# Optimization experiments

Measured on AMD Instinct MI355X. Metric: run time of the kernel, lower is better.

Reference implementation:

```python
import jax, jax.numpy as jnp
from jax import lax
import numpy as np

VTH = 1.0  # config['v_threshold']

@jax.custom_vjp
def mg_spike(x):
    # forward of MultiGaussianSurrogate: Heaviside
    return (x > 0).astype(x.dtype)

def _mg_fwd(x):
    return mg_spike(x), x

def _mg_bwd(x, g):
    lens, scale, height, gamma = 0.5, 6.0, 0.15, 0.5
    def gaussian(v, mu, sigma):
        return jnp.exp(-(v - mu) ** 2 / (2.0 * sigma ** 2)) / jnp.sqrt(2.0 * jnp.pi) / sigma
    temp = (gaussian(x, 0.0, lens) * (1.0 + height)
            - gaussian(x, lens, scale * lens) * height
            - gaussian(x, -lens, scale * lens) * height)
    return (g * temp * gamma,)

mg_spike.defvjp(_mg_fwd, _mg_bwd)

def setup_inputs():
    key = jax.random.key(0)
    ks = jax.random.split(key, 6)
    B, T, D, H, O = 256, 250, 700, 1024, 35
    x = jax.random.normal(ks[0], (B, T, D), dtype=jnp.float32)
    W_dense = jax.random.normal(ks[1], (D, H), dtype=jnp.float32) / np.sqrt(D).astype(np.float32)
    b_dense = jnp.zeros((H,), dtype=jnp.float32)
    W_out = jax.random.normal(ks[2], (H, O), dtype=jnp.float32) / np.sqrt(H).astype(np.float32)
    b_out = jnp.zeros((O,), dtype=jnp.float32)
    tau_m = jax.random.uniform(ks[3], (H,), dtype=jnp.float32, minval=0.0, maxval=4.0)
    mem0 = jax.random.uniform(ks[4], (B, H), dtype=jnp.float32)
    spike0 = jax.random.uniform(ks[5], (B, H), dtype=jnp.float32)
    return {"x": x, "W_dense": W_dense, "b_dense": b_dense,
            "W_out": W_out, "b_out": b_out, "tau_m": tau_m,
            "mem0": mem0, "spike0": spike0}

def reference(x, W_dense, b_dense, W_out, b_out, tau_m, mem0, spike0):
    B, T, D = x.shape
    O = W_out.shape[1]
    alpha = jax.nn.sigmoid(tau_m)  # [H], constant over time
    # batch the input projection once: [B,T,H] -> scan over T
    d_all = jnp.einsum('btd,dh->bth', x, W_dense) + b_dense
    d_all = jnp.swapaxes(d_all, 0, 1)  # [T,B,H]

    def step(carry, inp):
        mem, spike, acc = carry
        d_input, i = inp
        mem = mem * alpha + (1.0 - alpha) * d_input - VTH * spike
        spike = mg_spike(mem - VTH)
        probs = jax.nn.softmax(spike @ W_out + b_out, axis=1)  # [B,O]
        acc = acc + jnp.where(i > 10, probs, jnp.zeros_like(probs))
        return (mem, spike, acc), None

    acc0 = jnp.zeros((B, O), dtype=x.dtype)
    (_, _, out), _ = lax.scan(step, (mem0, spike0, acc0), (d_all, jnp.arange(T)))
    return out
```

## Files before the change

### kernel.cpp

```cpp
#include <hip/hip_runtime.h>
#include <cstdint>
#include <cstddef>

#define B_ 256
#define T_ 250
#define D_ 700
#define KP 704
#define H_ 1024
#define O_ 35
#define NT 22
#define MPAD 256

typedef __attribute__((ext_vector_type(8))) short s16x8;
typedef __attribute__((ext_vector_type(4))) float fx4;

__device__ __forceinline__ unsigned short f2bf(float v) {
    union { float f; unsigned int u; } a; a.f = v;
    unsigned int r = a.u + 0x7FFFu + ((a.u >> 16) & 1u);
    return (unsigned short)(r >> 16);
}

__device__ __forceinline__ void glds16(const unsigned short* g, void* l) {
    __builtin_amdgcn_global_load_lds(
        (const __attribute__((address_space(1))) unsigned int*)(const void*)g,
        (__attribute__((address_space(3))) unsigned int*)l, 16, 0, 0);
}

__global__ __launch_bounds__(256)
void convW(const float* __restrict__ Wd, unsigned short* __restrict__ WhT,
           unsigned short* __restrict__ WlT)
{
    __shared__ float tile[32][33];
    const int tx = threadIdx.x, ty = threadIdx.y;
    const int bx = blockIdx.x, by = blockIdx.y;
#pragma unroll
    for (int i = 0; i < 4; ++i) {
        int k = by * 32 + ty + i * 8;
        int n = bx * 32 + tx;
        tile[ty + i * 8][tx] = (k < D_) ? Wd[(size_t)k * H_ + n] : 0.f;
    }
    __syncthreads();
#pragma unroll
    for (int i = 0; i < 4; ++i) {
        int n = bx * 32 + ty + i * 8;
        int k = by * 32 + tx;
        float v = tile[tx][ty + i * 8];
        unsigned short h = f2bf(v);
        union { unsigned int u; float f; } hf; hf.u = ((unsigned int)h) << 16;
        unsigned short lo = f2bf(v - hf.f);
        WhT[(size_t)n * KP + k] = h;
        WlT[(size_t)n * KP + k] = lo;
    }
}

__global__ __launch_bounds__(256)
void convX(const float* __restrict__ X, unsigned short* __restrict__ xh,
           unsigned short* __restrict__ xl)
{
    int idx = blockIdx.x * 256 + threadIdx.x;
    if (idx >= B_ * T_ * 88) return;
    int m = idx / 88, s = idx - m * 88;
    int k = s * 8;
    int b = m / T_, tt = m - b * T_;
    const float* row = X + (size_t)m * D_;
    float v[8];
#pragma unroll
    for (int j = 0; j < 4; ++j) v[j] = row[k + j];
    if (k + 4 < D_) {
#pragma unroll
        for (int j = 0; j < 4; ++j) v[4 + j] = row[k + 4 + j];
    } else {
#pragma unroll
        for (int j = 0; j < 4; ++j) v[4 + j] = 0.f;
    }
    unsigned int hw[4], lw[4];
#pragma unroll
    for (int j = 0; j < 4; ++j) {
        unsigned short h0 = f2bf(v[2 * j]), h1 = f2bf(v[2 * j + 1]);
        union { unsigned int u; float f; } a0, a1;
        a0.u = ((unsigned int)h0) << 16; a1.u = ((unsigned int)h1) << 16;
        unsigned short l0 = f2bf(v[2 * j] - a0.f), l1 = f2bf(v[2 * j + 1] - a1.f);
        hw[j] = (unsigned int)h0 | ((unsigned int)h1 << 16);
        lw[j] = (unsigned int)l0 | ((unsigned int)l1 << 16);
    }
    size_t drow = (size_t)(b * MPAD + tt) * KP + k;
    *reinterpret_cast<uint4*>(xh + drow) = make_uint4(hw[0], hw[1], hw[2], hw[3]);
    *reinterpret_cast<uint4*>(xl + drow) = make_uint4(lw[0], lw[1], lw[2], lw[3]);
}

__global__ __launch_bounds__(512, 2)
void gemm1(const unsigned short* __restrict__ Ahp, const unsigned short* __restrict__ Alp,
           const unsigned short* __restrict__ Bhp, const unsigned short* __restrict__ Blp,
           const float* __restrict__ bias, const float* __restrict__ tau,
           const float* __restrict__ mem0, const float* __restrict__ spk0,
           unsigned long long* __restrict__ bits)
{
    extern __shared__ char smem[];
    const int tid = threadIdx.x;
    const int l = tid & 63, w = tid >> 6;
    const int wm = w >> 2, wn = w & 3;

    const int nwg = gridDim.x, orig = blockIdx.x;
    const int xcd = orig & 7, idx = orig >> 3;
    const int q = nwg >> 3, r = nwg & 7;
    const int swz = (xcd < r ? xcd * (q + 1) : r * (q + 1) + (xcd - r) * q) + idx;
    const int by = swz >> 2, bx = swz & 3;
    const int m0 = by * MPAD, n0 = bx * 256;

    const int rr = tid >> 2, ss = tid & 3;
    const int sw8 = ((ss ^ ((rr >> 1) & 3)) << 3);
    const int offA = (m0 + rr) * KP + sw8;
    const int offB = (n0 + rr) * KP + sw8;
    const int wbase = w * 1024;

    const int ra0 = wm * 128 + (l & 15);
    const int rb0 = wn * 64 + (l & 15);
    const int aHb = ra0 * 64 + (((l >> 4) ^ ((ra0 >> 1) & 3)) << 4);
    const int bHb = rb0 * 64 + (((l >> 4) ^ ((rb0 >> 1) & 3)) << 4);

    fx4 acc[8][4];
#pragma unroll
    for (int i = 0; i < 8; ++i)
#pragma unroll
        for (int j = 0; j < 4; ++j) acc[i][j] = (fx4)0.f;

    auto stageA = [&](int buf, int t) {
        char* base = smem + buf * 65536 + wbase;
        const int k = t * 32;
        glds16(Ahp + offA + k, base);
        glds16(Ahp + offA + 128 * KP + k, base + 8192);
        glds16(Alp + offA + k, base + 16384);
        glds16(Alp + offA + 128 * KP + k, base + 24576);
    };
    auto stageB = [&](int buf, int t) {
        char* base = smem + buf * 65536 + 32768 + wbase;
        const int k = t * 32;
        glds16(Bhp + offB + k, base);
        glds16(Bhp + offB + 128 * KP + k, base + 8192);
        glds16(Blp + offB + k, base + 16384);
        glds16(Blp + offB + 128 * KP + k, base + 24576);
    };

    stageA(0, 0);
    stageB(0, 0);
    stageB(1, 1);
    asm volatile("s_waitcnt vmcnt(4)" ::: "memory");
    __builtin_amdgcn_s_barrier();

    for (int t = 0; t < NT; ++t) {
        const char* cb = smem + (t & 1) * 65536;
        s16x8 ah0[4], al0[4], ah1[4], al1[4], bh[4], bl[4];

#pragma unroll
        for (int f = 0; f < 4; ++f) {
            ah0[f] = *(const s16x8*)(cb + aHb + f * 1024);
            bh[f]  = *(const s16x8*)(cb + 32768 + bHb + f * 1024);
        }
        if (t + 1 < NT) stageA((t + 1) & 1, t + 1);

#pragma unroll
        for (int f = 0; f < 4; ++f) {
            al0[f] = *(const s16x8*)(cb + 16384 + aHb + f * 1024);
            bl[f]  = *(const s16x8*)(cb + 49152 + bHb + f * 1024);
        }
        __builtin_amdgcn_s_setprio(1);
#pragma unroll
        for (int fm = 0; fm < 4; ++fm)
#pragma unroll
            for (int fn = 0; fn < 4; ++fn)
                acc[fm][fn] = __builtin_amdgcn_mfma_f32_16x16x32_bf16(ah0[fm], bh[fn], acc[fm][fn], 0, 0, 0);
        __builtin_amdgcn_s_setprio(0);

#pragma unroll
        for (int f = 0; f < 4; ++f) {
            ah1[f] = *(const s16x8*)(cb + aHb + 4096 + f * 1024);
            al1[f] = *(const s16x8*)(cb + 16384 + aHb + 4096 + f * 1024);
        }
        __builtin_amdgcn_s_setprio(1);
#pragma unroll
        for (int fm = 0; fm < 4; ++fm)
#pragma unroll
            for (int fn = 0; fn < 4; ++fn) {
                acc[fm][fn] = __builtin_amdgcn_mfma_f32_16x16x32_bf16(ah0[fm], bl[fn], acc[fm][fn], 0, 0, 0);
                acc[fm][fn] = __builtin_amdgcn_mfma_f32_16x16x32_bf16(al0[fm], bh[fn], acc[fm][fn], 0, 0, 0);
            }
        __builtin_amdgcn_s_setprio(0);
        __builtin_amdgcn_sched_barrier(0);
        __builtin_amdgcn_s_barrier();

        if (t + 2 < NT) {
            stageB(t & 1, t + 2);
            asm volatile("s_waitcnt vmcnt(4)" ::: "memory");
        } else {
            asm volatile("s_waitcnt vmcnt(0)" ::: "memory");
        }

        __builtin_amdgcn_s_setprio(1);
#pragma unroll
        for (int fm = 0; fm < 4; ++fm)
#pragma unroll
            for (int fn = 0; fn < 4; ++fn)
                acc[fm + 4][fn] = __builtin_amdgcn_mfma_f32_16x16x32_bf16(ah1[fm], bh[fn], acc[fm + 4][fn], 0, 0, 0);
        __builtin_amdgcn_s_setprio(0);

        __builtin_amdgcn_s_setprio(1);
#pragma unroll
        for (int fm = 0; fm < 4; ++fm)
#pragma unroll
            for (int fn = 0; fn < 4; ++fn) {
                acc[fm + 4][fn] = __builtin_amdgcn_mfma_f32_16x16x32_bf16(ah1[fm], bl[fn], acc[fm + 4][fn], 0, 0, 0);
                acc[fm + 4][fn] = __builtin_amdgcn_mfma_f32_16x16x32_bf16(al1[fm], bh[fn], acc[fm + 4][fn], 0, 0, 0);
            }
        __builtin_amdgcn_s_setprio(0);
        __builtin_amdgcn_sched_barrier(0);
        __builtin_amdgcn_s_barrier();
    }

    float bv[4];
#pragma unroll
    for (int fn = 0; fn < 4; ++fn) bv[fn] = bias[n0 + wn * 64 + fn * 16 + (l & 15)];

    float* dl = (float*)smem;
    const int bb = by;
    const int lane = tid & 63;

    float memv = 0.f, spkv = 0.f, alh = 0.f, omh = 0.f;
    unsigned long long* bp = nullptr;
    if (tid < 256) {
        const int h = n0 + tid;
        alh = 1.f / (1.f + expf(-tau[h]));
        omh = 1.f - alh;
        memv = mem0[bb * H_ + h];
        spkv = spk0[bb * H_ + h];
        bp = bits + (((size_t)bb * T_) << 4) + (h >> 6);
    }

#pragma unroll 1
    for (int ck = 0; ck < 2; ++ck) {
        __syncthreads();
        if (wm == ck) {
            const int colb = wn * 64;
#pragma unroll
            for (int fm = 0; fm < 8; ++fm) {
#pragma unroll
                for (int fn = 0; fn < 4; ++fn) {
                    int col = colb + fn * 16 + (l & 15);
#pragma unroll
                    for (int rg = 0; rg < 4; ++rg) {
                        int row = fm * 16 + (l >> 4) * 4 + rg;
                        dl[row * 256 + (col ^ (((row >> 2) & 1) << 4))] = acc[fm][fn][rg] + bv[fn];
                    }
                }
            }
        }
        __syncthreads();
        if (tid < 256) {
            const int nsteps = ck ? (T_ - 128) : 128;
            const int tbase = ck * 128;
            int ttl = 0;
            for (; ttl + 8 <= nsteps; ttl += 8) {
                float dr[8];
#pragma unroll
                for (int j = 0; j < 8; ++j) {
                    int rj = ttl + j;
                    dr[j] = dl[rj * 256 + (tid ^ (((rj >> 2) & 1) << 4))];
                }
#pragma unroll
                for (int j = 0; j < 8; ++j) {
                    memv = memv * alh + omh * dr[j] - spkv;
                    bool fire = (memv - 1.f) > 0.f;
                    spkv = fire ? 1.f : 0.f;
                    unsigned long long msk = __ballot(fire);
                    if (lane == 0) bp[(size_t)(tbase + ttl + j) << 4] = msk;
                }
            }
            for (; ttl < nsteps; ++ttl) {
                float d = dl[ttl * 256 + (tid ^ (((ttl >> 2) & 1) << 4))];
                memv = memv * alh + omh * d - spkv;
                bool fire = (memv - 1.f) > 0.f;
                spkv = fire ? 1.f : 0.f;
                unsigned long long msk = __ballot(fire);
                if (lane == 0) bp[(size_t)(tbase + ttl) << 4] = msk;
            }
        }
    }
}

__global__ __launch_bounds__(256)
void out_probs(const unsigned long long* __restrict__ bits,
               const float* __restrict__ Wo, const float* __restrict__ bo,
               float* __restrict__ probs)
{
    const int tid = threadIdx.x;
    const int r = blockIdx.x * 64 + (tid >> 2);
    const int q = tid & 3;
    const int b = r / 239, tt = r - b * 239;
    const int t = tt + 11;
    float lg[35];
#pragma unroll
    for (int o = 0; o < 35; ++o) lg[o] = (q == 0) ? bo[o] : 0.f;
    const unsigned long long* bp = bits + ((size_t)(b * T_ + t) << 4) + q * 4;
#pragma unroll
    for (int w2 = 0; w2 < 4; ++w2) {
        unsigned long long wb = bp[w2];
        const float* wbase = Wo + (size_t)((q * 4 + w2) * 64) * O_;
        while (wb) {
            int i = __builtin_ctzll(wb);
            wb &= wb - 1;
            const float* wr = wbase + i * O_;
#pragma unroll
            for (int o = 0; o < 35; ++o) lg[o] += wr[o];
        }
    }
#pragma unroll
    for (int o = 0; o < 35; ++o) lg[o] += __shfl_xor(lg[o], 1);
#pragma unroll
    for (int o = 0; o < 35; ++o) lg[o] += __shfl_xor(lg[o], 2);
    float mx = lg[0];
#pragma unroll
    for (int o = 1; o < 35; ++o) mx = fmaxf(mx, lg[o]);
    float sum = 0.f;
#pragma unroll
    for (int o = 0; o < 35; ++o) { lg[o] = expf(lg[o] - mx); sum += lg[o]; }
    float inv = 1.f / sum;
    float* pr = probs + (size_t)r * O_;
#pragma unroll
    for (int o = 0; o < 35; ++o) if (o / 9 == q) pr[o] = lg[o] * inv;
}

__global__ __launch_bounds__(256)
void acc_k(const float* __restrict__ probs, float* __restrict__ out)
{
    __shared__ float sp[64][36];
    const int b = blockIdx.x, tid = threadIdx.x;
    const int rl = tid >> 2, q = tid & 3;
    float a9[9];
#pragma unroll
    for (int j = 0; j < 9; ++j) a9[j] = 0.f;
    for (int c = 0; c < 239; c += 64) {
        int i = c + rl;
        if (i < 239) {
            const float* pr = probs + (size_t)(b * 239 + i) * O_ + q * 9;
#pragma unroll
            for (int j = 0; j < 9; ++j) if (j < 8 || q < 3) a9[j] += pr[j];
        }
    }
#pragma unroll
    for (int j = 0; j < 9; ++j) if (j < 8 || q < 3) sp[rl][q * 9 + j] = a9[j];
    __syncthreads();
    if (tid < 35) {
        float a = 0.f;
        for (int rr = 0; rr < 64; ++rr) a += sp[rr][tid];
        out[b * O_ + tid] = a;
    }
}

extern "C" void kernel_launch(void* const* d_in, const int* in_sizes, int n_in,
                              void* d_out, int out_size, void* d_ws, size_t ws_size,
                              hipStream_t stream) {
    const float* x    = (const float*)d_in[0];
    const float* Wd   = (const float*)d_in[1];
    const float* bd   = (const float*)d_in[2];
    const float* Wo   = (const float*)d_in[3];
    const float* bo   = (const float*)d_in[4];
    const float* tau  = (const float*)d_in[5];
    const float* mem0 = (const float*)d_in[6];
    const float* spk0 = (const float*)d_in[7];
    float* out = (float*)d_out;

    char* ws = (char*)d_ws;
    size_t off = 0;
    auto take = [&](size_t bytes) -> void* {
        void* p = ws + off;
        off = (off + bytes + 255) & ~(size_t)255;
        return p;
    };

    unsigned long long* bits = (unsigned long long*)take((size_t)B_ * T_ * 16 * 8);
    unsigned short* WhT = (unsigned short*)take((size_t)H_ * KP * 2);
    unsigned short* WlT = (unsigned short*)take((size_t)H_ * KP * 2);
    float* probs = (float*)take((size_t)B_ * 239 * O_ * 4);
    unsigned short* xh = (unsigned short*)take((size_t)B_ * MPAD * KP * 2);
    unsigned short* xl = (unsigned short*)take((size_t)B_ * MPAD * KP * 2);

    convW<<<dim3(32, 22), dim3(32, 8), 0, stream>>>(Wd, WhT, WlT);
    convX<<<(B_ * T_ * 88 + 255) / 256, 256, 0, stream>>>(x, xh, xl);
    gemm1<<<B_ * 4, 512, 131072, stream>>>(xh, xl, WhT, WlT, bd, tau, mem0, spk0, bits);
    out_probs<<<956, 256, 0, stream>>>(bits, Wo, bo, probs);
    acc_k<<<B_, 256, 0, stream>>>(probs, out);
}
```

Before: 338.1 us.

## Triple-buffer B tiles in gemm1 to remove mid-iteration barrier

Reorganizes gemm1's shared memory so the A tiles stay double-buffered while the B tiles become triple-buffered, raising dynamic LDS from 128KB to 160KB. The B prefetch for t+2 now goes into a third buffer, which removes the mid-iteration barrier, and the wait on loads moves to the top of each iteration. Launch bounds drop to one block per CU, since 160KB of LDS no longer fits two. The aim is to cut synchronization stalls and get more load/MFMA overlap, at the cost of lower occupancy.

Result: no change. 336.5 us, median of 2 (-0.5%).

```diff
diff --git a/kernel.cpp b/kernel.cpp
--- a/kernel.cpp
+++ b/kernel.cpp
@@ -88,7 +88,7 @@
     *reinterpret_cast<uint4*>(xl + drow) = make_uint4(lw[0], lw[1], lw[2], lw[3]);
 }
 
-__global__ __launch_bounds__(512, 2)
+__global__ __launch_bounds__(512, 1)
 void gemm1(const unsigned short* __restrict__ Ahp, const unsigned short* __restrict__ Alp,
            const unsigned short* __restrict__ Bhp, const unsigned short* __restrict__ Blp,
            const float* __restrict__ bias, const float* __restrict__ tau,
@@ -125,15 +125,15 @@
         for (int j = 0; j < 4; ++j) acc[i][j] = (fx4)0.f;
 
     auto stageA = [&](int buf, int t) {
-        char* base = smem + buf * 65536 + wbase;
+        char* base = smem + buf * 32768 + wbase;
         const int k = t * 32;
         glds16(Ahp + offA + k, base);
         glds16(Ahp + offA + 128 * KP + k, base + 8192);
         glds16(Alp + offA + k, base + 16384);
         glds16(Alp + offA + 128 * KP + k, base + 24576);
     };
-    auto stageB = [&](int buf, int t) {
-        char* base = smem + buf * 65536 + 32768 + wbase;
+    auto stageB = [&](int bufB, int t) {
+        char* base = smem + 65536 + bufB * 32768 + wbase;
         const int k = t * 32;
         glds16(Bhp + offB + k, base);
         glds16(Bhp + offB + 128 * KP + k, base + 8192);
@@ -141,27 +141,35 @@
         glds16(Blp + offB + 128 * KP + k, base + 24576);
     };
 
-    stageA(0, 0);
     stageB(0, 0);
     stageB(1, 1);
-    asm volatile("s_waitcnt vmcnt(4)" ::: "memory");
+    stageA(0, 0);
+    asm volatile("s_waitcnt vmcnt(0)" ::: "memory");
     __builtin_amdgcn_s_barrier();
 
     for (int t = 0; t < NT; ++t) {
-        const char* cb = smem + (t & 1) * 65536;
+        const char* ab = smem + (t & 1) * 32768;
+        const char* bb = smem + 65536 + (t % 3) * 32768;
         s16x8 ah0[4], al0[4], ah1[4], al1[4], bh[4], bl[4];
 
+        if (t + 1 < NT) {
+            asm volatile("s_waitcnt vmcnt(4)" ::: "memory");
+        } else {
+            asm volatile("s_waitcnt vmcnt(0)" ::: "memory");
+        }
+        __builtin_amdgcn_sched_barrier(0);
+
 #pragma unroll
         for (int f = 0; f < 4; ++f) {
-            ah0[f] = *(const s16x8*)(cb + aHb + f * 1024);
-            bh[f]  = *(const s16x8*)(cb + 32768 + bHb + f * 1024);
+            ah0[f] = *(const s16x8*)(ab + aHb + f * 1024);
+            bh[f]  = *(const s16x8*)(bb + bHb + f * 1024);
         }
         if (t + 1 < NT) stageA((t + 1) & 1, t + 1);
 
 #pragma unroll
         for (int f = 0; f < 4; ++f) {
-            al0[f] = *(const s16x8*)(cb + 16384 + aHb + f * 1024);
-            bl[f]  = *(const s16x8*)(cb + 49152 + bHb + f * 1024);
+            al0[f] = *(const s16x8*)(ab + 16384 + aHb + f * 1024);
+            bl[f]  = *(const s16x8*)(bb + 16384 + bHb + f * 1024);
         }
         __builtin_amdgcn_s_setprio(1);
 #pragma unroll
@@ -173,8 +181,8 @@
 
 #pragma unroll
         for (int f = 0; f < 4; ++f) {
-            ah1[f] = *(const s16x8*)(cb + aHb + 4096 + f * 1024);
-            al1[f] = *(const s16x8*)(cb + 16384 + aHb + 4096 + f * 1024);
+            ah1[f] = *(const s16x8*)(ab + aHb + 4096 + f * 1024);
+            al1[f] = *(const s16x8*)(ab + 16384 + aHb + 4096 + f * 1024);
         }
         __builtin_amdgcn_s_setprio(1);
 #pragma unroll
@@ -186,14 +194,8 @@
             }
         __builtin_amdgcn_s_setprio(0);
         __builtin_amdgcn_sched_barrier(0);
-        __builtin_amdgcn_s_barrier();
-
-        if (t + 2 < NT) {
-            stageB(t & 1, t + 2);
-            asm volatile("s_waitcnt vmcnt(4)" ::: "memory");
-        } else {
-            asm volatile("s_waitcnt vmcnt(0)" ::: "memory");
-        }
+
+        if (t + 2 < NT) stageB((t + 2) % 3, t + 2);
 
         __builtin_amdgcn_s_setprio(1);
 #pragma unroll
@@ -221,7 +223,7 @@
     for (int fn = 0; fn < 4; ++fn) bv[fn] = bias[n0 + wn * 64 + fn * 16 + (l & 15)];
 
     float* dl = (float*)smem;
-    const int bb = by;
+    const int bb2 = by;
     const int lane = tid & 63;
 
     float memv = 0.f, spkv = 0.f, alh = 0.f, omh = 0.f;
@@ -230,9 +232,9 @@
         const int h = n0 + tid;
         alh = 1.f / (1.f + expf(-tau[h]));
         omh = 1.f - alh;
-        memv = mem0[bb * H_ + h];
-        spkv = spk0[bb * H_ + h];
-        bp = bits + (((size_t)bb * T_) << 4) + (h >> 6);
+        memv = mem0[bb2 * H_ + h];
+        spkv = spk0[bb2 * H_ + h];
+        bp = bits + (((size_t)bb2 * T_) << 4) + (h >> 6);
     }
 
 #pragma unroll 1
@@ -383,9 +385,12 @@
     unsigned short* xh = (unsigned short*)take((size_t)B_ * MPAD * KP * 2);
     unsigned short* xl = (unsigned short*)take((size_t)B_ * MPAD * KP * 2);
 
+    (void)hipFuncSetAttribute((const void*)gemm1,
+                              hipFuncAttributeMaxDynamicSharedMemorySize, 163840);
+
     convW<<<dim3(32, 22), dim3(32, 8), 0, stream>>>(Wd, WhT, WlT);
     convX<<<(B_ * T_ * 88 + 255) / 256, 256, 0, stream>>>(x, xh, xl);
-    gemm1<<<B_ * 4, 512, 131072, stream>>>(xh, xl, WhT, WlT, bd, tau, mem0, spk0, bits);
+    gemm1<<<B_ * 4, 512, 163840, stream>>>(xh, xl, WhT, WlT, bd, tau, mem0, spk0, bits);
     out_probs<<<956, 256, 0, stream>>>(bits, Wo, bo, probs);
     acc_k<<<B_, 256, 0, stream>>>(probs, out);
 }
```
